# Performance work log

Measured on AMD Instinct MI355X. Metric: run time of the kernel, lower is better.

Reference implementation:

```python
import jax, jax.numpy as jnp
import numpy as np

N = 512          # hidden size n
B = 256          # batch
T = 512          # timesteps
INPUT_SIZE = 2
RANK = 2
ALPHA = 0.2
SIGMA_IN = 0.2
SIGMA_REC = 0.15


def setup_inputs() -> dict:
    key = jax.random.key(0)
    k1, k2, k3, k4, k5, k6 = jax.random.split(key, 6)
    u = jax.random.normal(k1, (B, T, INPUT_SIZE), dtype=jnp.float32)
    # standard normal; scaled by sqrt(2/alpha*sigma_in^2) inside reference
    input_noise = jax.random.normal(k2, (B, T, INPUT_SIZE), dtype=jnp.float32)
    # in the repo this is sigma_rec * randn projected on PCs; plain scaled randn here
    recurrent_noise = SIGMA_REC * jax.random.normal(k3, (B, T, N), dtype=jnp.float32)
    # low-rank recurrent weight: W_rec = A @ B, entries ~ U(-0.1, 0.1)
    A = 0.1 * (2.0 * jax.random.uniform(k4, (N, RANK), dtype=jnp.float32) - 1.0)
    Bm = 0.1 * (2.0 * jax.random.uniform(k5, (RANK, N), dtype=jnp.float32) - 1.0)
    W_rec = A @ Bm
    b_rec = jnp.zeros((N,), dtype=jnp.float32)  # normal_(std=0) -> zeros
    # nn.Linear default init: U(-1/sqrt(in), 1/sqrt(in))
    bound = 1.0 / np.sqrt(INPUT_SIZE)
    W_in = jax.random.uniform(k6, (N, INPUT_SIZE), dtype=jnp.float32,
                              minval=-bound, maxval=bound)
    return {"u": u, "input_noise": input_noise, "recurrent_noise": recurrent_noise,
            "W_in": W_in, "W_rec": W_rec, "b_rec": b_rec}


def reference(u, input_noise, recurrent_noise, W_in, W_rec, b_rec):
    alpha = ALPHA
    in_scale = np.sqrt(2.0 / ALPHA * SIGMA_IN ** 2).astype(np.float32)
    # inputs = input_layer(u + input_noise)  -> [B, T, N]
    inputs = jnp.einsum('bti,ni->btn', u + in_scale * input_noise, W_in)
    # scan over first T-1 timesteps, time-major
    xs = (jnp.swapaxes(inputs, 0, 1)[:-1],          # [T-1, B, N]
          jnp.swapaxes(recurrent_noise, 0, 1)[:-1])  # [T-1, B, N]
    s0 = jnp.zeros((u.shape[0], W_rec.shape[0]), dtype=u.dtype)

    def step(s, x):
        inp_t, noise_t = x
        s_new = (1.0 - alpha) * s + alpha * (
            jax.nn.relu(s) @ W_rec.T + b_rec + inp_t + noise_t)
        return s_new, s_new

    _, ys = jax.lax.scan(step, s0, xs)              # [T-1, B, N]
    states = jnp.concatenate([s0[None], ys], axis=0)  # [T, B, N]
    return jnp.swapaxes(states, 0, 1)               # [B, T, N]
```

## Files before the change

kernel.cpp:

```cpp
#include <hip/hip_runtime.h>
#include <math.h>

#define NH 512
#define BATCH 256
#define TT 512
#define NSTEPS (TT - 1)
#define ALPHA 0.2f
#define OMA 0.8f
#define ISCALE 0.6324555320336759f


__device__ __forceinline__ float wave_reduce_sum(float v) {
#pragma unroll
    for (int m = 32; m >= 1; m >>= 1) v += __shfl_xor(v, m, 64);
    return v;
}

__device__ __forceinline__ unsigned long long enc_key(float v, int i) {
    return (((unsigned long long)__float_as_uint(v)) << 32) | (unsigned int)i;
}


__global__ void k_rownorm(const float* __restrict__ W, unsigned long long* key1,
                          float* __restrict__ rn) {
    const int i = blockIdx.x, tid = threadIdx.x;
    const float4* row = (const float4*)(W + (size_t)i * NH);
    float acc = 0.f;
#pragma unroll
    for (int r = 0; r < 2; ++r) {
        float4 v = row[tid + 64 * r];
        acc = fmaf(v.x, v.x, fmaf(v.y, v.y, fmaf(v.z, v.z, fmaf(v.w, v.w, acc))));
    }
    acc = wave_reduce_sum(acc);
    if (tid == 0) {
        rn[i] = acc;
        atomicMax(key1, enc_key(acc, i));
    }
}

__global__ void k_rowdot(const float* __restrict__ W, const unsigned long long* key1,
                         unsigned long long* key2, const float* __restrict__ rn,
                         float* __restrict__ dv) {
    const int i = blockIdx.x, tid = threadIdx.x;
    const int i1 = (int)(*key1 & 0xffffffffULL);
    const float4* rowi = (const float4*)(W + (size_t)i * NH);
    const float4* row1 = (const float4*)(W + (size_t)i1 * NH);
    float acc = 0.f;
#pragma unroll
    for (int r = 0; r < 2; ++r) {
        float4 a = rowi[tid + 64 * r];
        float4 b = row1[tid + 64 * r];
        acc = fmaf(a.x, b.x, fmaf(a.y, b.y, fmaf(a.z, b.z, fmaf(a.w, b.w, acc))));
    }
    acc = wave_reduce_sum(acc);
    if (tid == 0) {
        dv[i] = acc;
        float resid = rn[i] - acc * acc / rn[i1];
        if (i != i1) atomicMax(key2, enc_key(fmaxf(resid, 0.f), i));
    }
}

__global__ void k_computeP(const float* __restrict__ W, const unsigned long long* key1,
                           const unsigned long long* key2, const float* __restrict__ rn,
                           const float* __restrict__ dv, float* __restrict__ P) {
    const int n = blockIdx.x, tid = threadIdx.x;
    const int i1 = (int)(*key1 & 0xffffffffULL);
    const int i2 = (int)(*key2 & 0xffffffffULL);
    const float4* rown = (const float4*)(W + (size_t)n * NH);
    const float4* row1 = (const float4*)(W + (size_t)i1 * NH);
    const float4* row2 = (const float4*)(W + (size_t)i2 * NH);
    float t0 = 0.f, t1 = 0.f;
#pragma unroll
    for (int r = 0; r < 2; ++r) {
        float4 a = rown[tid + 64 * r];
        float4 b = row1[tid + 64 * r];
        float4 c = row2[tid + 64 * r];
        t0 = fmaf(a.x, b.x, fmaf(a.y, b.y, fmaf(a.z, b.z, fmaf(a.w, b.w, t0))));
        t1 = fmaf(a.x, c.x, fmaf(a.y, c.y, fmaf(a.z, c.z, fmaf(a.w, c.w, t1))));
    }
    t0 = wave_reduce_sum(t0);
    t1 = wave_reduce_sum(t1);
    if (tid == 0) {
        float g11 = rn[i1], g22 = rn[i2], g12 = dv[i2];
        float det = fmaf(g11, g22, -g12 * g12);
        float inv = 1.f / det;
        P[2 * n]     = ALPHA * ((g22 * t0 - g12 * t1) * inv);
        P[2 * n + 1] = ALPHA * ((g11 * t1 - g12 * t0) * inv);
    }
}

__launch_bounds__(64, 1)
__global__ void k_main(const float* __restrict__ u, const float* __restrict__ inoise,
                       const float* __restrict__ rnoise, const float* __restrict__ W_in,
                       const float* __restrict__ W, const float* __restrict__ b_rec,
                       const unsigned long long* key1, const unsigned long long* key2,
                       const float* __restrict__ P, float* __restrict__ out) {
    __shared__ float4 lds_x[TT / 2];
    const int b = blockIdx.x, lane = threadIdx.x;
    const int i1 = (int)(key1[0] & 0xffffffffULL);
    const int i2 = (int)(key2[0] & 0xffffffffULL);

    const float4* u4 = (const float4*)(u + (size_t)b * TT * 2);
    const float4* n4 = (const float4*)(inoise + (size_t)b * TT * 2);
#pragma unroll
    for (int r = 0; r < 4; ++r) {
        float4 a = u4[lane + 64 * r];
        float4 c = n4[lane + 64 * r];
        float4 x;
        x.x = fmaf(ISCALE, c.x, a.x);
        x.y = fmaf(ISCALE, c.y, a.y);
        x.z = fmaf(ISCALE, c.z, a.z);
        x.w = fmaf(ISCALE, c.w, a.w);
        lds_x[lane + 64 * r] = x;
    }
    __syncthreads();

    const int n0 = lane * 8;
    float aa0[8], aa1[8], q0[8], q1[8], w0[8], w1[8], cb[8], s[8];
#pragma unroll
    for (int j = 0; j < 8; ++j) {
        const int n = n0 + j;
        aa0[j] = P[2 * n];
        aa1[j] = P[2 * n + 1];
        q0[j] = W[(size_t)i1 * NH + n];
        q1[j] = W[(size_t)i2 * NH + n];
        w0[j] = ALPHA * W_in[2 * n];
        w1[j] = ALPHA * W_in[2 * n + 1];
        cb[j] = ALPHA * b_rec[n];
        s[j] = 0.f;
    }

    const float* nzb = rnoise + (size_t)b * TT * NH + n0;
    float* ob = out + (size_t)b * TT * NH + n0;

    float4 z = {0.f, 0.f, 0.f, 0.f};
    *(float4*)(ob) = z;
    *(float4*)(ob + 4) = z;

    constexpr int PD = 8;
    float4 bA[PD], bB[PD];
#pragma unroll
    for (int k = 0; k < PD; ++k) {
        bA[k] = *(const float4*)(nzb + (size_t)k * NH);
        bB[k] = *(const float4*)(nzb + (size_t)k * NH + 4);
    }

    const float2* lx = (const float2*)lds_x;

    for (int tb = 0; tb < NSTEPS; tb += PD) {
#pragma unroll
        for (int k = 0; k < PD; ++k) {
            const int t = tb + k;
            if (t >= NSTEPS) break;

            float2 x = lx[t];

            float nz[8];
            nz[0] = bA[k].x; nz[1] = bA[k].y; nz[2] = bA[k].z; nz[3] = bA[k].w;
            nz[4] = bB[k].x; nz[5] = bB[k].y; nz[6] = bB[k].z; nz[7] = bB[k].w;
            int tp = t + PD; if (tp > NSTEPS - 1) tp = NSTEPS - 1;
            bA[k] = *(const float4*)(nzb + (size_t)tp * NH);
            bB[k] = *(const float4*)(nzb + (size_t)tp * NH + 4);

            float p0 = 0.f, p1 = 0.f;
#pragma unroll
            for (int j = 0; j < 8; ++j) {
                float rs = fmaxf(s[j], 0.f);
                p0 = fmaf(rs, q0[j], p0);
                p1 = fmaf(rs, q1[j], p1);
            }
#pragma unroll
            for (int m = 32; m >= 1; m >>= 1) {
                p0 += __shfl_xor(p0, m, 64);
                p1 += __shfl_xor(p1, m, 64);
            }

#pragma unroll
            for (int j = 0; j < 8; ++j) {
                float v = fmaf(ALPHA, nz[j], cb[j]);
                v = fmaf(w0[j], x.x, v);
                v = fmaf(w1[j], x.y, v);
                v = fmaf(aa0[j], p0, v);
                v = fmaf(aa1[j], p1, v);
                s[j] = fmaf(OMA, s[j], v);
            }

            float4 oA = {s[0], s[1], s[2], s[3]};
            float4 oB = {s[4], s[5], s[6], s[7]};
            *(float4*)(ob + (size_t)(t + 1) * NH) = oA;
            *(float4*)(ob + (size_t)(t + 1) * NH + 4) = oB;
        }
    }
}


extern "C" void kernel_launch(void* const* d_in, const int* in_sizes, int n_in,
                              void* d_out, int out_size, void* d_ws, size_t ws_size,
                              hipStream_t stream) {
    const float* u      = (const float*)d_in[0];
    const float* inoise = (const float*)d_in[1];
    const float* rnoise = (const float*)d_in[2];
    const float* W_in   = (const float*)d_in[3];
    const float* W      = (const float*)d_in[4];
    const float* b_rec  = (const float*)d_in[5];
    float* out = (float*)d_out;

    char* ws = (char*)d_ws;
    unsigned long long* key1 = (unsigned long long*)(ws + 0);
    unsigned long long* key2 = (unsigned long long*)(ws + 8);
    float* rn = (float*)(ws + 64);
    float* dv = (float*)(ws + 2112);
    float* P  = (float*)(ws + 4160);

    hipMemsetAsync(d_ws, 0, 16, stream);
    hipLaunchKernelGGL(k_rownorm, dim3(NH), dim3(64), 0, stream, W, key1, rn);
    hipLaunchKernelGGL(k_rowdot, dim3(NH), dim3(64), 0, stream, W, key1, key2, rn, dv);
    hipLaunchKernelGGL(k_computeP, dim3(NH), dim3(64), 0, stream, W, key1, key2, rn, dv, P);
    hipLaunchKernelGGL(k_main, dim3(BATCH), dim3(64), 0, stream,
                       u, inoise, rnoise, W_in, W, b_rec, key1, key2, P, out);
}
```

Before: 558.1 us.

## Replace atomics with in-kernel argmax, DPP reductions, nontemporal stores, deeper prefetch

Drops the memset and the global atomicMax argmax. Each block now recomputes the pivot rows by a wave-wide scan over the row norms. In the serial recurrence loop the cross-lane sum uses DPP row operations plus readlane instead of shfl_xor. The non-recurrent terms are computed off the critical path, and the 8-element partial sums use a tree add. The noise prefetch depth goes from 8 to 12, and output stores are nontemporal. Together these aim to shorten the per-step latency chain, at the cost of a different summation order and more registers.

Result: faster. 469.1 us (-15.9%).

```diff
diff --git a/kernel.cpp b/kernel.cpp
--- a/kernel.cpp
+++ b/kernel.cpp
@@ -4,10 +4,13 @@
 #define NH 512
 #define BATCH 256
 #define TT 512
-#define NSTEPS (TT - 1)
+#define NSTEPS 511
 #define ALPHA 0.2f
 #define OMA 0.8f
 #define ISCALE 0.6324555320336759f
+#define PD 12
+
+typedef float vf4 __attribute__((ext_vector_type(4)));
 
 
 __device__ __forceinline__ float wave_reduce_sum(float v) {
@@ -20,9 +23,46 @@
     return (((unsigned long long)__float_as_uint(v)) << 32) | (unsigned int)i;
 }
 
-
-__global__ void k_rownorm(const float* __restrict__ W, unsigned long long* key1,
-                          float* __restrict__ rn) {
+__device__ __forceinline__ unsigned long long wave_max_key(unsigned long long k) {
+#pragma unroll
+    for (int m = 32; m >= 1; m >>= 1) {
+        unsigned long long o = __shfl_xor(k, m, 64);
+        k = (o > k) ? o : k;
+    }
+    return k;
+}
+
+__device__ __forceinline__ int scan_argmax_rn(const float* __restrict__ rn, int tid) {
+    const float4* rn4 = (const float4*)rn;
+    unsigned long long key = 0;
+#pragma unroll
+    for (int r = 0; r < 2; ++r) {
+        float4 v = rn4[tid + 64 * r];
+        int base = 4 * (tid + 64 * r);
+        unsigned long long k0 = enc_key(v.x, base);
+        unsigned long long k1 = enc_key(v.y, base + 1);
+        unsigned long long k2 = enc_key(v.z, base + 2);
+        unsigned long long k3 = enc_key(v.w, base + 3);
+        k0 = k0 > k1 ? k0 : k1;
+        k2 = k2 > k3 ? k2 : k3;
+        k0 = k0 > k2 ? k0 : k2;
+        key = key > k0 ? key : k0;
+    }
+    return (int)(wave_max_key(key) & 0xffffffffULL);
+}
+
+__device__ __forceinline__ float dpp_sum63(float v) {
+    v += __int_as_float(__builtin_amdgcn_update_dpp(0, __float_as_int(v), 0x111, 0xf, 0xf, true));
+    v += __int_as_float(__builtin_amdgcn_update_dpp(0, __float_as_int(v), 0x112, 0xf, 0xf, true));
+    v += __int_as_float(__builtin_amdgcn_update_dpp(0, __float_as_int(v), 0x114, 0xf, 0xf, true));
+    v += __int_as_float(__builtin_amdgcn_update_dpp(0, __float_as_int(v), 0x118, 0xf, 0xf, true));
+    v += __int_as_float(__builtin_amdgcn_update_dpp(0, __float_as_int(v), 0x142, 0xa, 0xf, true));
+    v += __int_as_float(__builtin_amdgcn_update_dpp(0, __float_as_int(v), 0x143, 0xc, 0xf, true));
+    return v;
+}
+
+
+__global__ void k_rownorm(const float* __restrict__ W, float* __restrict__ rn) {
     const int i = blockIdx.x, tid = threadIdx.x;
     const float4* row = (const float4*)(W + (size_t)i * NH);
     float acc = 0.f;
@@ -32,17 +72,13 @@
         acc = fmaf(v.x, v.x, fmaf(v.y, v.y, fmaf(v.z, v.z, fmaf(v.w, v.w, acc))));
     }
     acc = wave_reduce_sum(acc);
-    if (tid == 0) {
-        rn[i] = acc;
-        atomicMax(key1, enc_key(acc, i));
-    }
-}
-
-__global__ void k_rowdot(const float* __restrict__ W, const unsigned long long* key1,
-                         unsigned long long* key2, const float* __restrict__ rn,
+    if (tid == 0) rn[i] = acc;
+}
+
+__global__ void k_rowdot(const float* __restrict__ W, const float* __restrict__ rn,
                          float* __restrict__ dv) {
     const int i = blockIdx.x, tid = threadIdx.x;
-    const int i1 = (int)(*key1 & 0xffffffffULL);
+    const int i1 = scan_argmax_rn(rn, tid);
     const float4* rowi = (const float4*)(W + (size_t)i * NH);
     const float4* row1 = (const float4*)(W + (size_t)i1 * NH);
     float acc = 0.f;
@@ -53,19 +89,40 @@
         acc = fmaf(a.x, b.x, fmaf(a.y, b.y, fmaf(a.z, b.z, fmaf(a.w, b.w, acc))));
     }
     acc = wave_reduce_sum(acc);
-    if (tid == 0) {
-        dv[i] = acc;
-        float resid = rn[i] - acc * acc / rn[i1];
-        if (i != i1) atomicMax(key2, enc_key(fmaxf(resid, 0.f), i));
-    }
-}
-
-__global__ void k_computeP(const float* __restrict__ W, const unsigned long long* key1,
-                           const unsigned long long* key2, const float* __restrict__ rn,
-                           const float* __restrict__ dv, float* __restrict__ P) {
+    if (tid == 0) dv[i] = acc;
+}
+
+__global__ void k_computeP(const float* __restrict__ W, const float* __restrict__ rn,
+                           const float* __restrict__ dv, float* __restrict__ P,
+                           int* __restrict__ idx) {
     const int n = blockIdx.x, tid = threadIdx.x;
-    const int i1 = (int)(*key1 & 0xffffffffULL);
-    const int i2 = (int)(*key2 & 0xffffffffULL);
+    const int i1 = scan_argmax_rn(rn, tid);
+    const float rn1 = rn[i1];
+    const float inv1 = 1.f / rn1;
+
+    const float4* rn4 = (const float4*)rn;
+    const float4* dv4 = (const float4*)dv;
+    unsigned long long key = 0;
+#pragma unroll
+    for (int r = 0; r < 2; ++r) {
+        float4 a = rn4[tid + 64 * r];
+        float4 d = dv4[tid + 64 * r];
+        int base = 4 * (tid + 64 * r);
+        float r0 = fmaxf(a.x - d.x * d.x * inv1, 0.f);
+        float r1 = fmaxf(a.y - d.y * d.y * inv1, 0.f);
+        float r2 = fmaxf(a.z - d.z * d.z * inv1, 0.f);
+        float r3 = fmaxf(a.w - d.w * d.w * inv1, 0.f);
+        unsigned long long k0 = (base + 0 != i1) ? enc_key(r0, base + 0) : 0ULL;
+        unsigned long long k1 = (base + 1 != i1) ? enc_key(r1, base + 1) : 0ULL;
+        unsigned long long k2 = (base + 2 != i1) ? enc_key(r2, base + 2) : 0ULL;
+        unsigned long long k3 = (base + 3 != i1) ? enc_key(r3, base + 3) : 0ULL;
+        k0 = k0 > k1 ? k0 : k1;
+        k2 = k2 > k3 ? k2 : k3;
+        k0 = k0 > k2 ? k0 : k2;
+        key = key > k0 ? key : k0;
+    }
+    const int i2 = (int)(wave_max_key(key) & 0xffffffffULL);
+
     const float4* rown = (const float4*)(W + (size_t)n * NH);
     const float4* row1 = (const float4*)(W + (size_t)i1 * NH);
     const float4* row2 = (const float4*)(W + (size_t)i2 * NH);
@@ -81,11 +138,12 @@
     t0 = wave_reduce_sum(t0);
     t1 = wave_reduce_sum(t1);
     if (tid == 0) {
-        float g11 = rn[i1], g22 = rn[i2], g12 = dv[i2];
+        float g11 = rn1, g22 = rn[i2], g12 = dv[i2];
         float det = fmaf(g11, g22, -g12 * g12);
         float inv = 1.f / det;
         P[2 * n]     = ALPHA * ((g22 * t0 - g12 * t1) * inv);
         P[2 * n + 1] = ALPHA * ((g11 * t1 - g12 * t0) * inv);
+        if (n == 0) { idx[0] = i1; idx[1] = i2; }
     }
 }
 
@@ -93,15 +151,16 @@
 __global__ void k_main(const float* __restrict__ u, const float* __restrict__ inoise,
                        const float* __restrict__ rnoise, const float* __restrict__ W_in,
                        const float* __restrict__ W, const float* __restrict__ b_rec,
-                       const unsigned long long* key1, const unsigned long long* key2,
-                       const float* __restrict__ P, float* __restrict__ out) {
-    __shared__ float4 lds_x[TT / 2];
+                       const int* __restrict__ idx, const float* __restrict__ P,
+                       float* __restrict__ out) {
+    __shared__ float2 lds_x[TT];
     const int b = blockIdx.x, lane = threadIdx.x;
-    const int i1 = (int)(key1[0] & 0xffffffffULL);
-    const int i2 = (int)(key2[0] & 0xffffffffULL);
+    const int i1 = idx[0];
+    const int i2 = idx[1];
 
     const float4* u4 = (const float4*)(u + (size_t)b * TT * 2);
     const float4* n4 = (const float4*)(inoise + (size_t)b * TT * 2);
+    float4* lx4 = (float4*)lds_x;
 #pragma unroll
     for (int r = 0; r < 4; ++r) {
         float4 a = u4[lane + 64 * r];
@@ -111,7 +170,7 @@
         x.y = fmaf(ISCALE, c.y, a.y);
         x.z = fmaf(ISCALE, c.z, a.z);
         x.w = fmaf(ISCALE, c.w, a.w);
-        lds_x[lane + 64 * r] = x;
+        lx4[lane + 64 * r] = x;
     }
     __syncthreads();
 
@@ -133,11 +192,10 @@
     const float* nzb = rnoise + (size_t)b * TT * NH + n0;
     float* ob = out + (size_t)b * TT * NH + n0;
 
-    float4 z = {0.f, 0.f, 0.f, 0.f};
-    *(float4*)(ob) = z;
-    *(float4*)(ob + 4) = z;
-
-    constexpr int PD = 8;
+    vf4 z = {0.f, 0.f, 0.f, 0.f};
+    __builtin_nontemporal_store(z, (vf4*)ob);
+    __builtin_nontemporal_store(z, (vf4*)(ob + 4));
+
     float4 bA[PD], bB[PD];
 #pragma unroll
     for (int k = 0; k < PD; ++k) {
@@ -145,52 +203,56 @@
         bB[k] = *(const float4*)(nzb + (size_t)k * NH + 4);
     }
 
-    const float2* lx = (const float2*)lds_x;
-
-    for (int tb = 0; tb < NSTEPS; tb += PD) {
-#pragma unroll
-        for (int k = 0; k < PD; ++k) {
-            const int t = tb + k;
-            if (t >= NSTEPS) break;
-
-            float2 x = lx[t];
-
-            float nz[8];
-            nz[0] = bA[k].x; nz[1] = bA[k].y; nz[2] = bA[k].z; nz[3] = bA[k].w;
-            nz[4] = bB[k].x; nz[5] = bB[k].y; nz[6] = bB[k].z; nz[7] = bB[k].w;
-            int tp = t + PD; if (tp > NSTEPS - 1) tp = NSTEPS - 1;
-            bA[k] = *(const float4*)(nzb + (size_t)tp * NH);
-            bB[k] = *(const float4*)(nzb + (size_t)tp * NH + 4);
-
-            float p0 = 0.f, p1 = 0.f;
-#pragma unroll
-            for (int j = 0; j < 8; ++j) {
-                float rs = fmaxf(s[j], 0.f);
-                p0 = fmaf(rs, q0[j], p0);
-                p1 = fmaf(rs, q1[j], p1);
-            }
-#pragma unroll
-            for (int m = 32; m >= 1; m >>= 1) {
-                p0 += __shfl_xor(p0, m, 64);
-                p1 += __shfl_xor(p1, m, 64);
-            }
-
-#pragma unroll
-            for (int j = 0; j < 8; ++j) {
-                float v = fmaf(ALPHA, nz[j], cb[j]);
-                v = fmaf(w0[j], x.x, v);
-                v = fmaf(w1[j], x.y, v);
-                v = fmaf(aa0[j], p0, v);
-                v = fmaf(aa1[j], p1, v);
-                s[j] = fmaf(OMA, s[j], v);
-            }
-
-            float4 oA = {s[0], s[1], s[2], s[3]};
-            float4 oB = {s[4], s[5], s[6], s[7]};
-            *(float4*)(ob + (size_t)(t + 1) * NH) = oA;
-            *(float4*)(ob + (size_t)(t + 1) * NH + 4) = oB;
-        }
-    }
+#define STEP(t_, k_, REFILL_)                                                        \
+    {                                                                                \
+        const int t = (t_);                                                          \
+        float2 x = lds_x[t];                                                         \
+        float nz[8];                                                                 \
+        nz[0] = bA[k_].x; nz[1] = bA[k_].y; nz[2] = bA[k_].z; nz[3] = bA[k_].w;      \
+        nz[4] = bB[k_].x; nz[5] = bB[k_].y; nz[6] = bB[k_].z; nz[7] = bB[k_].w;      \
+        if (REFILL_) {                                                               \
+            int tp = t + PD; if (tp > NSTEPS) tp = NSTEPS;     \
+            bA[k_] = *(const float4*)(nzb + (size_t)tp * NH);                        \
+            bB[k_] = *(const float4*)(nzb + (size_t)tp * NH + 4);                    \
+        }                                                                            \
+        float base_[8], m0[8], m1[8];                                                \
+        _Pragma("unroll")                                                            \
+        for (int j = 0; j < 8; ++j) {                                                \
+            float rs = fmaxf(s[j], 0.f);                                             \
+            m0[j] = rs * q0[j];                                                      \
+            m1[j] = rs * q1[j];                                                      \
+            float v = fmaf(ALPHA, nz[j], cb[j]);                                     \
+            v = fmaf(w0[j], x.x, v);                                                 \
+            v = fmaf(w1[j], x.y, v);                                                 \
+            base_[j] = fmaf(OMA, s[j], v);                                           \
+        }                                                                            \
+        float a0 = ((m0[0] + m0[1]) + (m0[2] + m0[3])) +                             \
+                   ((m0[4] + m0[5]) + (m0[6] + m0[7]));                              \
+        float a1 = ((m1[0] + m1[1]) + (m1[2] + m1[3])) +                             \
+                   ((m1[4] + m1[5]) + (m1[6] + m1[7]));                              \
+        float r0 = dpp_sum63(a0);                                                    \
+        float r1 = dpp_sum63(a1);                                                    \
+        float p0 = __int_as_float(__builtin_amdgcn_readlane(__float_as_int(r0), 63));\
+        float p1 = __int_as_float(__builtin_amdgcn_readlane(__float_as_int(r1), 63));\
+        _Pragma("unroll")                                                            \
+        for (int j = 0; j < 8; ++j) {                                                \
+            float v = fmaf(aa0[j], p0, base_[j]);                                    \
+            s[j] = fmaf(aa1[j], p1, v);                                              \
+        }                                                                            \
+        vf4 oA = {s[0], s[1], s[2], s[3]};                                           \
+        vf4 oB = {s[4], s[5], s[6], s[7]};                                           \
+        __builtin_nontemporal_store(oA, (vf4*)(ob + (size_t)(t + 1) * NH));          \
+        __builtin_nontemporal_store(oB, (vf4*)(ob + (size_t)(t + 1) * NH + 4));      \
+    }
+
+    for (int tb = 0; tb < 504; tb += PD) {
+#pragma unroll
+        for (int k = 0; k < PD; ++k) STEP(tb + k, k, true)
+    }
+#pragma unroll
+    for (int k = 0; k < 7; ++k) STEP(504 + k, k, false)
+
+#undef STEP
 }
 
 
@@ -206,16 +268,14 @@
     float* out = (float*)d_out;
 
     char* ws = (char*)d_ws;
-    unsigned long long* key1 = (unsigned long long*)(ws + 0);
-    unsigned long long* key2 = (unsigned long long*)(ws + 8);
+    int* idx  = (int*)(ws + 0);
     float* rn = (float*)(ws + 64);
     float* dv = (float*)(ws + 2112);
     float* P  = (float*)(ws + 4160);
 
-    hipMemsetAsync(d_ws, 0, 16, stream);
-    hipLaunchKernelGGL(k_rownorm, dim3(NH), dim3(64), 0, stream, W, key1, rn);
-    hipLaunchKernelGGL(k_rowdot, dim3(NH), dim3(64), 0, stream, W, key1, key2, rn, dv);
-    hipLaunchKernelGGL(k_computeP, dim3(NH), dim3(64), 0, stream, W, key1, key2, rn, dv, P);
+    hipLaunchKernelGGL(k_rownorm, dim3(NH), dim3(64), 0, stream, W, rn);
+    hipLaunchKernelGGL(k_rowdot, dim3(NH), dim3(64), 0, stream, W, rn, dv);
+    hipLaunchKernelGGL(k_computeP, dim3(NH), dim3(64), 0, stream, W, rn, dv, P, idx);
     hipLaunchKernelGGL(k_main, dim3(BATCH), dim3(64), 0, stream,
-                       u, inoise, rnoise, W_in, W, b_rec, key1, key2, P, out);
-}
+                       u, inoise, rnoise, W_in, W, b_rec, idx, P, out);
+}
```
